# Kernel optimization log

Measured on AMD Instinct MI355X. Metric: run time of the kernel, lower is better.

The kernel has to match this reference:

```python
import jax, jax.numpy as jnp
import numpy as np

B, S, D = 2, 4096, 2048
H, DK = 16, 128          # num_heads, head_dim (DK == DV)
GATE_NORM = 16.0         # gate_logit_normalizer (GLA default)


def setup_inputs() -> dict:
    key = jax.random.key(0)
    ks = jax.random.split(key, 6)
    sc = 1.0 / np.sqrt(D)
    return {
        "x": jax.random.normal(ks[0], (B, S, D), dtype=jnp.float32),
        "Wq": jax.random.normal(ks[1], (D, D), dtype=jnp.float32) * sc,
        "Wk": jax.random.normal(ks[2], (D, D), dtype=jnp.float32) * sc,
        "Wv": jax.random.normal(ks[3], (D, D), dtype=jnp.float32) * sc,
        "Wg": jax.random.normal(ks[4], (D, D), dtype=jnp.float32) * sc,
        "Wo": jax.random.normal(ks[5], (D, D), dtype=jnp.float32) * sc,
    }


def _gla(q, k, v, gk):
    """Gated linear attention recurrence.
    q,k,gk: [B,H,S,DK]; v: [B,H,S,DV]. Returns o: [B,H,S,DV].
    S_t = diag(exp(gk_t)) @ S_{t-1} + k_t v_t^T;  o_t = q_t @ S_t.
    """
    def step(state, inp):
        q_t, k_t, v_t, g_t = inp  # each [B,H,DK] / [B,H,DV]
        state = state * jnp.exp(g_t)[..., None] + k_t[..., None] * v_t[..., None, :]
        o_t = jnp.einsum("bhk,bhkv->bhv", q_t, state)
        return state, o_t

    init = jnp.zeros((q.shape[0], q.shape[1], q.shape[3], v.shape[3]), q.dtype)
    # scan over time: move seq axis to front
    xs = tuple(jnp.moveaxis(t, 2, 0) for t in (q, k, v, gk))
    _, o = jax.lax.scan(step, init, xs)  # o: [S,B,H,DV]
    return jnp.moveaxis(o, 0, 2)


def reference(x, Wq, Wk, Wv, Wg, Wo):
    b, s, _ = x.shape
    split = lambda t: t.reshape(b, s, H, DK).transpose(0, 2, 1, 3)  # [B,H,S,DK]
    q = split(x @ Wq) * (DK ** -0.5)
    k = split(x @ Wk)
    v = split(x @ Wv)
    gk = jax.nn.log_sigmoid(split(x @ Wg)) / GATE_NORM  # data-dependent log decay
    o = _gla(q, k, v, gk)                                # [B,H,S,DV]
    o = o.transpose(0, 2, 1, 3).reshape(b, s, H * DK)
    return o @ Wo
```

## Files before the change

### kernel.cpp

```cpp
#include <hip/hip_runtime.h>
#include <hip/hip_bf16.h>

#define B_SZ 2
#define S_LEN 4096
#define D_MODEL 2048
#define NH 16
#define DKH 128
#define CHUNK 32
#define SEG 256
#define NSEG 16
#define NCH 8
#define GEMM_M 8192
#define GEMM_N 2048
#define GEMM_K 2048

typedef __bf16 bf16x8 __attribute__((ext_vector_type(8)));
typedef float f32x4 __attribute__((ext_vector_type(4)));
typedef unsigned short u16x4 __attribute__((ext_vector_type(4)));
typedef unsigned short u16x8 __attribute__((ext_vector_type(8)));

__device__ inline float bf2f(unsigned short u) {
  unsigned int x = ((unsigned int)u) << 16;
  return __builtin_bit_cast(float, x);
}
__device__ inline unsigned short f2bf(float f) {
  __hip_bfloat16 h = __float2bfloat16(f);
  return __builtin_bit_cast(unsigned short, h);
}
__device__ inline unsigned int packhl(float s) {
  unsigned short h = f2bf(s);
  unsigned short l = f2bf(s - bf2f(h));
  return ((unsigned int)h << 16) | (unsigned int)l;
}

__global__ __launch_bounds__(256) void cast_bf16_kernel(const float* __restrict__ in,
                                                        unsigned short* __restrict__ out,
                                                        int nvec8) {
  int i = blockIdx.x * 256 + threadIdx.x;
  if (i >= nvec8) return;
  const float4* p = (const float4*)in + (size_t)i * 2;
  float4 a = p[0], b = p[1];
  uint4 o;
  o.x = (unsigned)f2bf(a.x) | ((unsigned)f2bf(a.y) << 16);
  o.y = (unsigned)f2bf(a.z) | ((unsigned)f2bf(a.w) << 16);
  o.z = (unsigned)f2bf(b.x) | ((unsigned)f2bf(b.y) << 16);
  o.w = (unsigned)f2bf(b.z) | ((unsigned)f2bf(b.w) << 16);
  ((uint4*)out)[i] = o;
}

__global__ __launch_bounds__(256) void transpose_cast_kernel(const float* __restrict__ W,
                                                             unsigned short* __restrict__ Wt) {
  __shared__ float tile[64][65];
  const int n0 = blockIdx.x * 64, k0 = blockIdx.y * 64;
  for (int jj = 0; jj < 16; ++jj) {
    int flat = threadIdx.x + jj * 256;
    int r = flat >> 6, c = flat & 63;
    tile[r][c] = W[(size_t)(k0 + r) * D_MODEL + n0 + c];
  }
  __syncthreads();
  for (int jj = 0; jj < 16; ++jj) {
    int flat = threadIdx.x + jj * 256;
    int rr = flat >> 6, cc = flat & 63;
    Wt[(size_t)(n0 + rr) * D_MODEL + k0 + cc] = f2bf(tile[cc][rr]);
  }
}

__device__ inline void async16(void* lds_dst, const void* gsrc) {
  __builtin_amdgcn_global_load_lds((__attribute__((address_space(1))) void*)(void*)gsrc,
                                   (__attribute__((address_space(3))) void*)lds_dst,
                                   16, 0, 0);
}

template <int MODE>
__global__ __launch_bounds__(256) void gemm_bt(const unsigned short* __restrict__ A,
                                               const unsigned short* __restrict__ Bt,
                                               void* __restrict__ Cout) {
  __shared__ unsigned short As[128 * 32];
  __shared__ unsigned short Bs[128 * 32];
  const int tid = threadIdx.x;
  const int lane = tid & 63, w = tid >> 6;
  const int bm = blockIdx.y * 128, bn = blockIdx.x * 128;
  const int wm = w >> 1, wn = w & 1;
  const int lr = lane & 15, lg = lane >> 4;

  f32x4 acc[4][4] = {};

  const int srow = (lane >> 2);
  const int scol = (lane & 3) * 8;

  for (int kk = 0; kk < GEMM_K; kk += 32) {
    async16(&As[(w * 32 + 0) * 32],
            &A[(size_t)(bm + w * 32 + 0 + srow) * GEMM_K + kk + scol]);
    async16(&As[(w * 32 + 16) * 32],
            &A[(size_t)(bm + w * 32 + 16 + srow) * GEMM_K + kk + scol]);
    async16(&Bs[(w * 32 + 0) * 32],
            &Bt[(size_t)(bn + w * 32 + 0 + srow) * GEMM_K + kk + scol]);
    async16(&Bs[(w * 32 + 16) * 32],
            &Bt[(size_t)(bn + w * 32 + 16 + srow) * GEMM_K + kk + scol]);
    __syncthreads();

    bf16x8 af[4], bfr[4];
#pragma unroll
    for (int mi = 0; mi < 4; ++mi)
      af[mi] = *(const bf16x8*)&As[(wm * 64 + mi * 16 + lr) * 32 + lg * 8];
#pragma unroll
    for (int nj = 0; nj < 4; ++nj)
      bfr[nj] = *(const bf16x8*)&Bs[(wn * 64 + nj * 16 + lr) * 32 + lg * 8];
#pragma unroll
    for (int mi = 0; mi < 4; ++mi)
#pragma unroll
      for (int nj = 0; nj < 4; ++nj)
        acc[mi][nj] = __builtin_amdgcn_mfma_f32_16x16x32_bf16(af[mi], bfr[nj], acc[mi][nj], 0, 0, 0);
    __syncthreads();
  }

#pragma unroll
  for (int mi = 0; mi < 4; ++mi) {
#pragma unroll
    for (int nj = 0; nj < 4; ++nj) {
#pragma unroll
      for (int r = 0; r < 4; ++r) {
        int row = bm + wm * 64 + mi * 16 + lg * 4 + r;
        int col = bn + wn * 64 + nj * 16 + lr;
        float v = acc[mi][nj][r];
        size_t idx = (size_t)row * GEMM_N + col;
        if constexpr (MODE == 0) {
          ((unsigned short*)Cout)[idx] = f2bf(v);
        } else if constexpr (MODE == 1) {
          ((unsigned short*)Cout)[idx] = f2bf(v * 0.08838834764831845f);
        } else if constexpr (MODE == 2) {
          float ls = fminf(v, 0.f) - log1pf(expf(-fabsf(v)));
          ((unsigned short*)Cout)[idx] = f2bf(ls * 0.0625f);
        } else {
          ((float*)Cout)[idx] = v;
        }
      }
    }
  }
}

__global__ __launch_bounds__(256) void gla_seg1(
    const unsigned short* qb, const unsigned short* __restrict__ kb,
    const unsigned short* __restrict__ vb, const unsigned short* __restrict__ gkb,
    unsigned short* qhat, unsigned short* __restrict__ obuf,
    float* __restrict__ dS, float* __restrict__ Dseg) {
  __shared__ __align__(16) unsigned short rawq[32 * 128];
  __shared__ __align__(16) unsigned short rawk[32 * 128];
  __shared__ __align__(16) unsigned short rawv[32 * 128];
  __shared__ __align__(16) unsigned short rawg[32 * 128];
  __shared__ __align__(16) unsigned short qt[32 * 136];
  __shared__ __align__(16) unsigned short kt[32 * 136];
  __shared__ __align__(16) unsigned short ktT[128 * 40];
  __shared__ __align__(16) unsigned short vT[128 * 40];
  __shared__ __align__(16) unsigned short Am[32 * 40];
  __shared__ __align__(16) unsigned short Shi[128 * 136];
  __shared__ __align__(16) unsigned short Slo[128 * 136];
  __shared__ __align__(16) float EGC[128];

  const int tid = threadIdx.x;
  const int lane = tid & 63, w = tid >> 6;
  const int lr = lane & 15, lg = lane >> 4;
  const int seg = blockIdx.x, h = blockIdx.y, b = blockIdx.z;
  const int colQ = h * DKH;
  const size_t segtok = (size_t)b * S_LEN + (size_t)seg * SEG;

  f32x4 sacc[2][8] = {};
  float gseg = 0.f;

  auto stage_chunk = [&](int c) {
    const size_t ctok = segtok + c * CHUNK;
    const int r0 = 8 * w;
    const int rr = r0 + (lane >> 4);
    const int cc = (lane & 15) * 8;
    async16(&rawq[(r0) * 128], &qb[(ctok + rr) * D_MODEL + colQ + cc]);
    async16(&rawq[(r0 + 4) * 128], &qb[(ctok + rr + 4) * D_MODEL + colQ + cc]);
    async16(&rawk[(r0) * 128], &kb[(ctok + rr) * D_MODEL + colQ + cc]);
    async16(&rawk[(r0 + 4) * 128], &kb[(ctok + rr + 4) * D_MODEL + colQ + cc]);
    async16(&rawv[(r0) * 128], &vb[(ctok + rr) * D_MODEL + colQ + cc]);
    async16(&rawv[(r0 + 4) * 128], &vb[(ctok + rr + 4) * D_MODEL + colQ + cc]);
    async16(&rawg[(r0) * 128], &gkb[(ctok + rr) * D_MODEL + colQ + cc]);
    async16(&rawg[(r0 + 4) * 128], &gkb[(ctok + rr + 4) * D_MODEL + colQ + cc]);
  };

  stage_chunk(0);

  for (int c = 0; c < NCH; ++c) {
    const size_t ctok = segtok + c * CHUNK;
    __syncthreads();

#pragma unroll
    for (int ktl = 0; ktl < 2; ++ktl) {
      const int k0 = 32 * w + ktl * 16 + lg * 4;
#pragma unroll
      for (int vt = 0; vt < 8; ++vt) {
        const int v = vt * 16 + lr;
        u16x4 hv, lv;
#pragma unroll
        for (int r = 0; r < 4; ++r) {
          float s = sacc[ktl][vt][r];
          unsigned short h_ = f2bf(s);
          hv[r] = h_;
          lv[r] = f2bf(s - bf2f(h_));
        }
        *(u16x4*)&Shi[v * 136 + k0] = hv;
        *(u16x4*)&Slo[v * 136 + k0] = lv;
      }
    }

    if (tid < 128) {
      const int k = tid;
      float g = 0.f;
      const float egsp = __expf(gseg);
#pragma unroll
      for (int t = 0; t < CHUNK; ++t) {
        g += bf2f(rawg[t * 128 + k]);
        float eg = __expf(g), ieg = __expf(-g);
        float qv = bf2f(rawq[t * 128 + k]) * eg;
        qt[t * 136 + k] = f2bf(qv);
        qhat[(ctok + t) * D_MODEL + colQ + k] = f2bf(qv * egsp);
        unsigned short kbf = f2bf(bf2f(rawk[t * 128 + k]) * ieg);
        kt[t * 136 + k] = kbf;
        ktT[k * 40 + t] = kbf;
      }
      EGC[k] = __expf(g);
      gseg += g;
    } else {
      const int j = tid - 128;
#pragma unroll
      for (int i = 0; i < 4; ++i) {
        int f = j * 4 + i;
        int t = f >> 4, v0 = (f & 15) * 8;
        u16x8 r8 = *(const u16x8*)&rawv[t * 128 + v0];
#pragma unroll
        for (int e = 0; e < 8; ++e) vT[(v0 + e) * 40 + t] = r8[e];
      }
    }
    __syncthreads();

    if (c + 1 < NCH) stage_chunk(c + 1);

    {
      const int tt = w >> 1, tpt = w & 1;
      if (tpt <= tt) {
        f32x4 aacc = {};
#pragma unroll
        for (int ks = 0; ks < 4; ++ks) {
          bf16x8 qa = *(const bf16x8*)&qt[(tt * 16 + lr) * 136 + ks * 32 + lg * 8];
          bf16x8 ka = *(const bf16x8*)&kt[(tpt * 16 + lr) * 136 + ks * 32 + lg * 8];
          aacc = __builtin_amdgcn_mfma_f32_16x16x32_bf16(qa, ka, aacc, 0, 0, 0);
        }
#pragma unroll
        for (int r = 0; r < 4; ++r) {
          int t = tt * 16 + lg * 4 + r;
          int tp = tpt * 16 + lr;
          Am[t * 40 + tp] = f2bf((tp <= t) ? aacc[r] : 0.f);
        }
      } else {
#pragma unroll
        for (int r = 0; r < 4; ++r) Am[(lg * 4 + r) * 40 + 16 + lr] = 0;
      }
    }
    __syncthreads();

    f32x4 oacc[2][2] = {};
#pragma unroll
    for (int ks = 0; ks < 4; ++ks) {
      bf16x8 qa0 = *(const bf16x8*)&qt[(lr) * 136 + ks * 32 + lg * 8];
      bf16x8 qa1 = *(const bf16x8*)&qt[(16 + lr) * 136 + ks * 32 + lg * 8];
#pragma unroll
      for (int vtl = 0; vtl < 2; ++vtl) {
        const int v = (2 * w + vtl) * 16 + lr;
        bf16x8 bh = *(const bf16x8*)&Shi[v * 136 + ks * 32 + lg * 8];
        bf16x8 bl = *(const bf16x8*)&Slo[v * 136 + ks * 32 + lg * 8];
        oacc[0][vtl] = __builtin_amdgcn_mfma_f32_16x16x32_bf16(qa0, bh, oacc[0][vtl], 0, 0, 0);
        oacc[0][vtl] = __builtin_amdgcn_mfma_f32_16x16x32_bf16(qa0, bl, oacc[0][vtl], 0, 0, 0);
        oacc[1][vtl] = __builtin_amdgcn_mfma_f32_16x16x32_bf16(qa1, bh, oacc[1][vtl], 0, 0, 0);
        oacc[1][vtl] = __builtin_amdgcn_mfma_f32_16x16x32_bf16(qa1, bl, oacc[1][vtl], 0, 0, 0);
      }
    }
    {
      bf16x8 am0 = *(const bf16x8*)&Am[(lr) * 40 + lg * 8];
      bf16x8 am1 = *(const bf16x8*)&Am[(16 + lr) * 40 + lg * 8];
#pragma unroll
      for (int vtl = 0; vtl < 2; ++vtl) {
        const int v = (2 * w + vtl) * 16 + lr;
        bf16x8 bv = *(const bf16x8*)&vT[v * 40 + lg * 8];
        oacc[0][vtl] = __builtin_amdgcn_mfma_f32_16x16x32_bf16(am0, bv, oacc[0][vtl], 0, 0, 0);
        oacc[1][vtl] = __builtin_amdgcn_mfma_f32_16x16x32_bf16(am1, bv, oacc[1][vtl], 0, 0, 0);
      }
    }
#pragma unroll
    for (int tt = 0; tt < 2; ++tt)
#pragma unroll
      for (int vtl = 0; vtl < 2; ++vtl) {
        const int v = (2 * w + vtl) * 16 + lr;
#pragma unroll
        for (int r = 0; r < 4; ++r)
          obuf[(ctok + tt * 16 + lg * 4 + r) * D_MODEL + colQ + v] = f2bf(oacc[tt][vtl][r]);
      }
    {
      bf16x8 ak0 = *(const bf16x8*)&ktT[(32 * w + lr) * 40 + lg * 8];
      bf16x8 ak1 = *(const bf16x8*)&ktT[(32 * w + 16 + lr) * 40 + lg * 8];
#pragma unroll
      for (int vt = 0; vt < 8; ++vt) {
        bf16x8 bv = *(const bf16x8*)&vT[(vt * 16 + lr) * 40 + lg * 8];
        sacc[0][vt] = __builtin_amdgcn_mfma_f32_16x16x32_bf16(ak0, bv, sacc[0][vt], 0, 0, 0);
        sacc[1][vt] = __builtin_amdgcn_mfma_f32_16x16x32_bf16(ak1, bv, sacc[1][vt], 0, 0, 0);
      }
      f32x4 eg0 = *(const f32x4*)&EGC[32 * w + lg * 4];
      f32x4 eg1 = *(const f32x4*)&EGC[32 * w + 16 + lg * 4];
#pragma unroll
      for (int vt = 0; vt < 8; ++vt) {
        sacc[0][vt] *= eg0;
        sacc[1][vt] *= eg1;
      }
    }
  }

  const size_t dsbase = (((size_t)(b * NH + h) * NSEG + seg) * 128) * 128;
#pragma unroll
  for (int ktl = 0; ktl < 2; ++ktl) {
    const int k0 = 32 * w + ktl * 16 + lg * 4;
#pragma unroll
    for (int vt = 0; vt < 8; ++vt) {
      const int v = vt * 16 + lr;
      float4 st;
      st.x = sacc[ktl][vt][0]; st.y = sacc[ktl][vt][1];
      st.z = sacc[ktl][vt][2]; st.w = sacc[ktl][vt][3];
      *(float4*)&dS[dsbase + (size_t)v * 128 + k0] = st;
    }
  }
  if (tid < 128) Dseg[((size_t)(b * NH + h) * NSEG + seg) * 128 + tid] = __expf(gseg);
}

__global__ __launch_bounds__(256) void gla_scan(float* dS, const float* __restrict__ Dseg) {
  unsigned int* Spk = (unsigned int*)dS;
  const int tid = threadIdx.x;
  const int vs = blockIdx.x, h = blockIdx.y, b = blockIdx.z;
  const int v = vs * 16 + (tid >> 4);
  const int k0 = (tid & 15) * 8;
  const size_t bh = (size_t)b * NH + h;
  float s[8];
#pragma unroll
  for (int j = 0; j < 8; ++j) s[j] = 0.f;

  for (int sg = 0; sg < NSEG; ++sg) {
    const size_t base = ((bh * NSEG + sg) * 128 + v) * 128 + k0;
    float4 x0 = *(const float4*)&dS[base];
    float4 x1 = *(const float4*)&dS[base + 4];
    const size_t dbase = (bh * NSEG + sg) * 128 + k0;
    float4 d0 = *(const float4*)&Dseg[dbase];
    float4 d1 = *(const float4*)&Dseg[dbase + 4];

    uint4 p0, p1;
    p0.x = packhl(s[0]); p0.y = packhl(s[1]); p0.z = packhl(s[2]); p0.w = packhl(s[3]);
    p1.x = packhl(s[4]); p1.y = packhl(s[5]); p1.z = packhl(s[6]); p1.w = packhl(s[7]);
    *(uint4*)&Spk[base] = p0;
    *(uint4*)&Spk[base + 4] = p1;

    s[0] = d0.x * s[0] + x0.x; s[1] = d0.y * s[1] + x0.y;
    s[2] = d0.z * s[2] + x0.z; s[3] = d0.w * s[3] + x0.w;
    s[4] = d1.x * s[4] + x1.x; s[5] = d1.y * s[5] + x1.y;
    s[6] = d1.z * s[6] + x1.z; s[7] = d1.w * s[7] + x1.w;
  }
}

__global__ __launch_bounds__(256) void gla_corr(const unsigned short* __restrict__ qhat,
                                                const unsigned int* __restrict__ Spk,
                                                unsigned short* __restrict__ obuf) {
  __shared__ __align__(16) unsigned short Sh[128 * 136];
  __shared__ __align__(16) unsigned short Sl[128 * 136];
  const int tid = threadIdx.x;
  const int lane = tid & 63, w = tid >> 6;
  const int lr = lane & 15, lg = lane >> 4;
  const int seg = blockIdx.x, h = blockIdx.y, b = blockIdx.z;
  const int colQ = h * DKH;
  const size_t segtok = (size_t)b * S_LEN + (size_t)seg * SEG;
  const size_t sbase = (((size_t)(b * NH + h) * NSEG + seg) * 128) * 128;

#pragma unroll
  for (int i = 0; i < 16; ++i) {
    int f = tid + i * 256;
    int v = f >> 5, k0 = (f & 31) * 4;
    uint4 p = *(const uint4*)&Spk[sbase + (size_t)v * 128 + k0];
    u16x4 hv, lv;
    hv[0] = (unsigned short)(p.x >> 16); lv[0] = (unsigned short)(p.x & 0xffff);
    hv[1] = (unsigned short)(p.y >> 16); lv[1] = (unsigned short)(p.y & 0xffff);
    hv[2] = (unsigned short)(p.z >> 16); lv[2] = (unsigned short)(p.z & 0xffff);
    hv[3] = (unsigned short)(p.w >> 16); lv[3] = (unsigned short)(p.w & 0xffff);
    *(u16x4*)&Sh[v * 136 + k0] = hv;
    *(u16x4*)&Sl[v * 136 + k0] = lv;
  }
  __syncthreads();

  for (int nt = 0; nt < 4; ++nt) {
    const int ttile = w * 4 + nt;
    const int t = ttile * 16 + lr;
    f32x4 acc8[8];
#pragma unroll
    for (int vt = 0; vt < 8; ++vt) {
      u16x4 c4 = *(const u16x4*)&obuf[(segtok + t) * D_MODEL + colQ + vt * 16 + lg * 4];
      acc8[vt][0] = bf2f(c4[0]); acc8[vt][1] = bf2f(c4[1]);
      acc8[vt][2] = bf2f(c4[2]); acc8[vt][3] = bf2f(c4[3]);
    }
#pragma unroll
    for (int ks = 0; ks < 4; ++ks) {
      bf16x8 bq = *(const bf16x8*)&qhat[(segtok + t) * D_MODEL + colQ + ks * 32 + lg * 8];
#pragma unroll
      for (int vt = 0; vt < 8; ++vt) {
        bf16x8 ah = *(const bf16x8*)&Sh[(vt * 16 + lr) * 136 + ks * 32 + lg * 8];
        bf16x8 al = *(const bf16x8*)&Sl[(vt * 16 + lr) * 136 + ks * 32 + lg * 8];
        acc8[vt] = __builtin_amdgcn_mfma_f32_16x16x32_bf16(ah, bq, acc8[vt], 0, 0, 0);
        acc8[vt] = __builtin_amdgcn_mfma_f32_16x16x32_bf16(al, bq, acc8[vt], 0, 0, 0);
      }
    }
#pragma unroll
    for (int vt = 0; vt < 8; ++vt) {
      u16x4 pk;
#pragma unroll
      for (int r = 0; r < 4; ++r) pk[r] = f2bf(acc8[vt][r]);
      *(u16x4*)&obuf[(segtok + t) * D_MODEL + colQ + vt * 16 + lg * 4] = pk;
    }
  }
}

extern "C" void kernel_launch(void* const* d_in, const int* in_sizes, int n_in,
                              void* d_out, int out_size, void* d_ws, size_t ws_size,
                              hipStream_t stream) {
  const float* x = (const float*)d_in[0];
  const float* W[5] = {(const float*)d_in[1], (const float*)d_in[2], (const float*)d_in[3],
                       (const float*)d_in[4], (const float*)d_in[5]};
  float* out = (float*)d_out;
  char* ws = (char*)d_ws;

  const size_t XBN = (size_t)B_SZ * S_LEN * D_MODEL;
  const size_t DD = (size_t)D_MODEL * D_MODEL;
  const size_t NSTATE = (size_t)B_SZ * NH * NSEG * 128 * 128;

  size_t off = 0;
  unsigned short* xb = (unsigned short*)(ws + off); off += XBN * 2;
  unsigned short* Wt = (unsigned short*)(ws + off); off += 5 * DD * 2;
  unsigned short* qb = (unsigned short*)(ws + off); off += XBN * 2;
  unsigned short* kb = (unsigned short*)(ws + off); off += XBN * 2;
  unsigned short* vb = (unsigned short*)(ws + off); off += XBN * 2;
  unsigned short* gkb = (unsigned short*)(ws + off); off += XBN * 2;
  float* dS = (float*)(ws + off); off += NSTATE * 4;
  float* Dsg = (float*)(ws + off); off += (size_t)B_SZ * NH * NSEG * 128 * 4;
  unsigned short* obuf = xb;

  cast_bf16_kernel<<<dim3((unsigned)(XBN / 8 / 256)), dim3(256), 0, stream>>>(x, xb, (int)(XBN / 8));
  for (int i = 0; i < 5; ++i)
    transpose_cast_kernel<<<dim3(32, 32), dim3(256), 0, stream>>>(W[i], Wt + (size_t)i * DD);

  dim3 gg(GEMM_N / 128, GEMM_M / 128);
  gemm_bt<1><<<gg, 256, 0, stream>>>(xb, Wt + 0 * DD, (void*)qb);
  gemm_bt<0><<<gg, 256, 0, stream>>>(xb, Wt + 1 * DD, (void*)kb);
  gemm_bt<0><<<gg, 256, 0, stream>>>(xb, Wt + 2 * DD, (void*)vb);
  gemm_bt<2><<<gg, 256, 0, stream>>>(xb, Wt + 3 * DD, (void*)gkb);

  gla_seg1<<<dim3(NSEG, NH, B_SZ), 256, 0, stream>>>(qb, kb, vb, gkb, qb , obuf, dS, Dsg);
  gla_scan<<<dim3(8, NH, B_SZ), 256, 0, stream>>>(dS, Dsg);
  gla_corr<<<dim3(NSEG, NH, B_SZ), 256, 0, stream>>>(qb , (const unsigned int*)dS, obuf);

  gemm_bt<3><<<gg, 256, 0, stream>>>(obuf, Wt + 4 * DD, (void*)out);
}
```

Before: 823.6 us.

## Replace 128x128 GEMM with double-buffered 256x256 swizzled-LDS GEMM

Replaces the 128x128-tile single-buffered bf16 GEMM with a 256x256 tile, 512-thread kernel using K-step 64, double-buffered async global-to-LDS loads with explicit vmcnt waits, XOR-swizzled LDS layout, and block-index swizzling for L2 locality. It aims to cut global traffic per FLOP, LDS bank conflicts, and the barrier stalls of the old load-then-compute loop. The larger LDS footprint (128KB per block) and higher register use reduce occupancy, and the grid shrinks to 256 blocks, which may leave some CUs underused.

After: 704.2 us. 1.17x faster.

```diff
diff --git a/kernel.cpp b/kernel.cpp
--- a/kernel.cpp
+++ b/kernel.cpp
@@ -13,6 +13,7 @@
 #define GEMM_M 8192
 #define GEMM_N 2048
 #define GEMM_K 2048
+#define NKT 32
 
 typedef __bf16 bf16x8 __attribute__((ext_vector_type(8)));
 typedef float f32x4 __attribute__((ext_vector_type(4)));
@@ -65,62 +66,98 @@
   }
 }
 
-__device__ inline void async16(void* lds_dst, const void* gsrc) {
+__device__ __forceinline__ void async16(void* lds_dst, const void* gsrc) {
   __builtin_amdgcn_global_load_lds((__attribute__((address_space(1))) void*)(void*)gsrc,
                                    (__attribute__((address_space(3))) void*)lds_dst,
                                    16, 0, 0);
 }
 
+__device__ __forceinline__ void memfence_compiler() { asm volatile("" ::: "memory"); }
+
+__device__ __forceinline__ void stage_tile(const unsigned short* __restrict__ G,
+                                           int row0, int k0,
+                                           unsigned short* lds_buf, int tid) {
+  const int r = tid >> 3;
+  const int ssw = ((tid & 7) ^ (r & 7)) * 8;
+  const unsigned short* src = &G[(size_t)(row0 + r) * GEMM_K + k0 + ssw];
+  char* dst = (char*)lds_buf + (tid >> 6) * 1024;
+#pragma unroll
+  for (int j = 0; j < 4; ++j)
+    async16(dst + j * 8192, src + (size_t)j * 64 * GEMM_K);
+}
+
 template <int MODE>
-__global__ __launch_bounds__(256) void gemm_bt(const unsigned short* __restrict__ A,
-                                               const unsigned short* __restrict__ Bt,
-                                               void* __restrict__ Cout) {
-  __shared__ unsigned short As[128 * 32];
-  __shared__ unsigned short Bs[128 * 32];
+__global__ __launch_bounds__(512, 2) void gemm256(const unsigned short* __restrict__ A,
+                                                  const unsigned short* __restrict__ Bt,
+                                                  void* __restrict__ Cout) {
+  __shared__ unsigned short As[2][256 * 64];
+  __shared__ unsigned short Bs[2][256 * 64];
   const int tid = threadIdx.x;
-  const int lane = tid & 63, w = tid >> 6;
-  const int bm = blockIdx.y * 128, bn = blockIdx.x * 128;
-  const int wm = w >> 1, wn = w & 1;
+  const int lane = tid & 63;
+  const int wid = tid >> 6;
+  const int wm = wid >> 2, wn = wid & 3;
   const int lr = lane & 15, lg = lane >> 4;
 
-  f32x4 acc[4][4] = {};
-
-  const int srow = (lane >> 2);
-  const int scol = (lane & 3) * 8;
-
-  for (int kk = 0; kk < GEMM_K; kk += 32) {
-    async16(&As[(w * 32 + 0) * 32],
-            &A[(size_t)(bm + w * 32 + 0 + srow) * GEMM_K + kk + scol]);
-    async16(&As[(w * 32 + 16) * 32],
-            &A[(size_t)(bm + w * 32 + 16 + srow) * GEMM_K + kk + scol]);
-    async16(&Bs[(w * 32 + 0) * 32],
-            &Bt[(size_t)(bn + w * 32 + 0 + srow) * GEMM_K + kk + scol]);
-    async16(&Bs[(w * 32 + 16) * 32],
-            &Bt[(size_t)(bn + w * 32 + 16 + srow) * GEMM_K + kk + scol]);
-    __syncthreads();
-
-    bf16x8 af[4], bfr[4];
-#pragma unroll
-    for (int mi = 0; mi < 4; ++mi)
-      af[mi] = *(const bf16x8*)&As[(wm * 64 + mi * 16 + lr) * 32 + lg * 8];
-#pragma unroll
-    for (int nj = 0; nj < 4; ++nj)
-      bfr[nj] = *(const bf16x8*)&Bs[(wn * 64 + nj * 16 + lr) * 32 + lg * 8];
-#pragma unroll
-    for (int mi = 0; mi < 4; ++mi)
+  const int lid = blockIdx.y * 8 + blockIdx.x;
+  const int swz = (lid & 7) * 32 + (lid >> 3);
+  const int bm = (swz >> 3) * 256;
+  const int bn = (swz & 7) * 256;
+
+  f32x4 acc[8][4] = {};
+
+  stage_tile(A, bm, 0, As[0], tid);
+  stage_tile(Bt, bn, 0, Bs[0], tid);
+  stage_tile(A, bm, 64, As[1], tid);
+  stage_tile(Bt, bn, 64, Bs[1], tid);
+  asm volatile("s_waitcnt vmcnt(8)" ::: "memory");
+  __builtin_amdgcn_s_barrier();
+  __builtin_amdgcn_sched_barrier(0);
+  memfence_compiler();
+
+  for (int t = 0; t < NKT; ++t) {
+    const int cur = t & 1;
+    const unsigned short* Ac = As[cur];
+    const unsigned short* Bc = Bs[cur];
+#pragma unroll
+    for (int ks = 0; ks < 2; ++ks) {
+      bf16x8 av[8], bv[4];
+      const int slot = ((ks << 2) | lg) ^ (lr & 7);
+#pragma unroll
+      for (int mi = 0; mi < 8; ++mi)
+        av[mi] = *(const bf16x8*)&Ac[(wm * 128 + mi * 16 + lr) * 64 + slot * 8];
 #pragma unroll
       for (int nj = 0; nj < 4; ++nj)
-        acc[mi][nj] = __builtin_amdgcn_mfma_f32_16x16x32_bf16(af[mi], bfr[nj], acc[mi][nj], 0, 0, 0);
-    __syncthreads();
-  }
-
-#pragma unroll
-  for (int mi = 0; mi < 4; ++mi) {
+        bv[nj] = *(const bf16x8*)&Bc[(wn * 64 + nj * 16 + lr) * 64 + slot * 8];
+      __builtin_amdgcn_s_setprio(1);
+#pragma unroll
+      for (int mi = 0; mi < 8; ++mi)
+#pragma unroll
+        for (int nj = 0; nj < 4; ++nj)
+          acc[mi][nj] = __builtin_amdgcn_mfma_f32_16x16x32_bf16(av[mi], bv[nj], acc[mi][nj], 0, 0, 0);
+      __builtin_amdgcn_s_setprio(0);
+    }
+    memfence_compiler();
+    __builtin_amdgcn_s_barrier();
+    __builtin_amdgcn_sched_barrier(0);
+    if (t + 2 < NKT) {
+      stage_tile(A, bm, (t + 2) * 64, As[cur], tid);
+      stage_tile(Bt, bn, (t + 2) * 64, Bs[cur], tid);
+      asm volatile("s_waitcnt vmcnt(8)" ::: "memory");
+    } else {
+      asm volatile("s_waitcnt vmcnt(0)" ::: "memory");
+    }
+    __builtin_amdgcn_s_barrier();
+    __builtin_amdgcn_sched_barrier(0);
+    memfence_compiler();
+  }
+
+#pragma unroll
+  for (int mi = 0; mi < 8; ++mi) {
 #pragma unroll
     for (int nj = 0; nj < 4; ++nj) {
 #pragma unroll
       for (int r = 0; r < 4; ++r) {
-        int row = bm + wm * 64 + mi * 16 + lg * 4 + r;
+        int row = bm + wm * 128 + mi * 16 + lg * 4 + r;
         int col = bn + wn * 64 + nj * 16 + lr;
         float v = acc[mi][nj][r];
         size_t idx = (size_t)row * GEMM_N + col;
@@ -452,15 +489,15 @@
   for (int i = 0; i < 5; ++i)
     transpose_cast_kernel<<<dim3(32, 32), dim3(256), 0, stream>>>(W[i], Wt + (size_t)i * DD);
 
-  dim3 gg(GEMM_N / 128, GEMM_M / 128);
-  gemm_bt<1><<<gg, 256, 0, stream>>>(xb, Wt + 0 * DD, (void*)qb);
-  gemm_bt<0><<<gg, 256, 0, stream>>>(xb, Wt + 1 * DD, (void*)kb);
-  gemm_bt<0><<<gg, 256, 0, stream>>>(xb, Wt + 2 * DD, (void*)vb);
-  gemm_bt<2><<<gg, 256, 0, stream>>>(xb, Wt + 3 * DD, (void*)gkb);
+  dim3 gg(GEMM_N / 256, GEMM_M / 256);
+  gemm256<1><<<gg, 512, 0, stream>>>(xb, Wt + 0 * DD, (void*)qb);
+  gemm256<0><<<gg, 512, 0, stream>>>(xb, Wt + 1 * DD, (void*)kb);
+  gemm256<0><<<gg, 512, 0, stream>>>(xb, Wt + 2 * DD, (void*)vb);
+  gemm256<2><<<gg, 512, 0, stream>>>(xb, Wt + 3 * DD, (void*)gkb);
 
   gla_seg1<<<dim3(NSEG, NH, B_SZ), 256, 0, stream>>>(qb, kb, vb, gkb, qb , obuf, dS, Dsg);
   gla_scan<<<dim3(8, NH, B_SZ), 256, 0, stream>>>(dS, Dsg);
   gla_corr<<<dim3(NSEG, NH, B_SZ), 256, 0, stream>>>(qb , (const unsigned int*)dS, obuf);
 
-  gemm_bt<3><<<gg, 256, 0, stream>>>(obuf, Wt + 4 * DD, (void*)out);
-}
+  gemm256<3><<<gg, 512, 0, stream>>>(obuf, Wt + 4 * DD, (void*)out);
+}
```
